# Performance work log

Measured on AMD Instinct MI355X. Metric: run time of the kernel, lower is better.

Reference implementation:

```python
import jax, jax.numpy as jnp
import numpy as np

N, NF, D, H, L, FFN, E, EF = 2048, 64, 256, 8, 6, 1024, 32768, 16
HD = D // H
MAXDEG, MAXDIST = 64, 8


def setup_inputs() -> dict:
    key = jax.random.key(0)
    ks = jax.random.split(key, 32)
    s = 0.02
    nrm = lambda k, sh: (jax.random.normal(k, sh, jnp.float32) * s)
    return {
        "x": jax.random.normal(ks[0], (N, NF), jnp.float32),
        "edge_attr": jax.random.normal(ks[1], (E, EF), jnp.float32),
        "node_proj_w": nrm(ks[2], (D, NF)),
        "node_proj_b": jnp.zeros((D,), jnp.float32),
        "in_deg_emb": nrm(ks[3], (MAXDEG + 1, D)),
        "out_deg_emb": nrm(ks[4], (MAXDEG + 1, D)),
        "dist_bias": nrm(ks[5], (MAXDIST + 2, H)),
        "edge_proj_w": nrm(ks[6], (H, EF)),
        "edge_proj_b": jnp.zeros((H,), jnp.float32),
        "cls_token": nrm(ks[7], (1, D)),
        "q_w": nrm(ks[8], (L, D, D)), "q_b": jnp.zeros((L, D)),
        "k_w": nrm(ks[9], (L, D, D)), "k_b": jnp.zeros((L, D)),
        "v_w": nrm(ks[10], (L, D, D)), "v_b": jnp.zeros((L, D)),
        "o_w": nrm(ks[11], (L, D, D)), "o_b": jnp.zeros((L, D)),
        "ffn1_w": nrm(ks[12], (L, FFN, D)), "ffn1_b": jnp.zeros((L, FFN)),
        "ffn2_w": nrm(ks[13], (L, D, FFN)), "ffn2_b": jnp.zeros((L, D)),
        "ln1_s": jnp.ones((L, D)), "ln1_b": jnp.zeros((L, D)),
        "ln2_s": jnp.ones((L, D)), "ln2_b": jnp.zeros((L, D)),
        "fn_s": jnp.ones((D,)), "fn_b": jnp.zeros((D,)),
        "edge_index": jax.random.randint(ks[14], (2, E), 0, N, dtype=jnp.int32),
        "dist_matrix": jax.random.randint(ks[15], (N, N), 0, MAXDIST + 2, dtype=jnp.int32),
    }


def _ln(v, s, b):
    m = v.mean(-1, keepdims=True)
    va = v.var(-1, keepdims=True)
    return (v - m) / jnp.sqrt(va + 1e-5) * s + b


def _forward(x, edge_attr, node_proj_w, node_proj_b, in_deg_emb, out_deg_emb,
             dist_bias, edge_proj_w, edge_proj_b, cls_token,
             q_w, q_b, k_w, k_b, v_w, v_b, o_w, o_b,
             ffn1_w, ffn1_b, ffn2_w, ffn2_b,
             ln1_s, ln1_b, ln2_s, ln2_b, fn_s, fn_b,
             edge_index, dist_matrix):
    # node embedding + degree encoding
    h = x @ node_proj_w.T + node_proj_b  # (N, D)
    ones = jnp.ones((E,), jnp.int32)
    in_deg = jnp.clip(jax.ops.segment_sum(ones, edge_index[1], num_segments=N), 0, MAXDEG)
    out_deg = jnp.clip(jax.ops.segment_sum(ones, edge_index[0], num_segments=N), 0, MAXDEG)
    h = h + in_deg_emb[in_deg] + out_deg_emb[out_deg]
    h = jnp.concatenate([cls_token, h], axis=0)  # (N+1, D), CLS at row 0
    Nf = N + 1
    # spatial bias: pad dist matrix with zeros for CLS, then embed
    dist_p = jnp.pad(jnp.clip(dist_matrix, 0, MAXDIST + 1), ((1, 0), (1, 0)))
    bias = dist_bias[dist_p]  # (Nf, Nf, H)
    # edge-feature bias: scatter-add projected edge features into dense (N,N,H)
    proj = edge_attr @ edge_proj_w.T + edge_proj_b  # (E, H)
    ebias = jnp.zeros((N, N, H), h.dtype).at[edge_index[0], edge_index[1]].add(proj)
    bias = bias + jnp.pad(ebias, ((1, 0), (1, 0), (0, 0)))
    bias_t = bias.transpose(2, 0, 1)  # (H, Nf, Nf)
    scale = np.sqrt(HD).astype(np.float32)
    for l in range(L):
        hn = _ln(h, ln1_s[l], ln1_b[l])
        Q = (hn @ q_w[l].T + q_b[l]).reshape(Nf, H, HD).transpose(1, 0, 2)
        K = (hn @ k_w[l].T + k_b[l]).reshape(Nf, H, HD).transpose(1, 0, 2)
        V = (hn @ v_w[l].T + v_b[l]).reshape(Nf, H, HD).transpose(1, 0, 2)
        logits = jnp.einsum('hnd,hmd->hnm', Q, K) / scale + bias_t
        attn = jax.nn.softmax(logits, axis=-1)
        o = jnp.einsum('hnm,hmd->hnd', attn, V).transpose(1, 0, 2).reshape(Nf, D)
        h = h + o @ o_w[l].T + o_b[l]
        hn2 = _ln(h, ln2_s[l], ln2_b[l])
        h = h + jax.nn.gelu(hn2 @ ffn1_w[l].T + ffn1_b[l], approximate=False) @ ffn2_w[l].T + ffn2_b[l]
    h = _ln(h, fn_s, fn_b)
    return h, h[0]


def reference(x, edge_attr, node_proj_w, node_proj_b, in_deg_emb, out_deg_emb,
              dist_bias, edge_proj_w, edge_proj_b, cls_token,
              q_w, q_b, k_w, k_b, v_w, v_b, o_w, o_b,
              ffn1_w, ffn1_b, ffn2_w, ffn2_b,
              ln1_s, ln1_b, ln2_s, ln2_b, fn_s, fn_b,
              edge_index, dist_matrix):
    return _forward(x, edge_attr, node_proj_w, node_proj_b, in_deg_emb, out_deg_emb,
                    dist_bias, edge_proj_w, edge_proj_b, cls_token,
                    q_w, q_b, k_w, k_b, v_w, v_b, o_w, o_b,
                    ffn1_w, ffn1_b, ffn2_w, ffn2_b,
                    ln1_s, ln1_b, ln2_s, ln2_b, fn_s, fn_b,
                    edge_index, dist_matrix)
```

## Files before the change

### kernel.cpp

```cpp
#include <hip/hip_runtime.h>
#include <math.h>

#define N_ 2048
#define NF_IN 64
#define D_ 256
#define H_ 8
#define HD_ 32
#define L_ 6
#define FFN_ 1024
#define E_ 32768
#define EF_ 16
#define NF 2049
#define MAXDEG_ 64
#define BSTRIDE 2112
#define RPAD 2112
#define NSPLIT 4
#define LOG2E 1.4426950408889634f

typedef __attribute__((ext_vector_type(8))) short bf16x8;
typedef __attribute__((ext_vector_type(4))) float f32x4;

__device__ inline unsigned short f2b(float f){
  union { float f; unsigned u; } v; v.f = f;
  unsigned r = (v.u + 0x7fffu + ((v.u >> 16) & 1u)) >> 16;
  return (unsigned short)r;
}
__device__ inline float b2f(short s){
  union { unsigned u; float f; } v; v.u = ((unsigned)(unsigned short)s) << 16;
  return v.f;
}

__device__ inline unsigned char f2fp8(float f){
  unsigned u = __float_as_uint(f);
  unsigned s = (u >> 24) & 0x80u;
  float a = fabsf(f);
  if (a >= 448.f) return (unsigned char)(s | 0x7Eu);
  if (a < 0.015625f){
    int k = (int)rintf(a * 512.f);
    return (unsigned char)(s | (unsigned)k);
  }
  int e; float m = frexpf(a, &e);
  int E = e - 1;
  int m3 = (int)rintf(m * 16.f) - 8;
  if (m3 == 8){ E++; m3 = 0; }
  if (E > 8){ E = 8; m3 = 6; }
  if (E == 8 && m3 > 6) m3 = 6;
  return (unsigned char)(s | (unsigned)((E + 7) << 3) | (unsigned)m3);
}
__device__ inline float fp82f(unsigned char b){
  return __builtin_amdgcn_cvt_f32_fp8((int)b, 0);
}

__device__ inline void atomic_add_fp8(unsigned char* p, float add){
  unsigned* wp = (unsigned*)((size_t)p & ~(size_t)3);
  int sh = (int)((size_t)p & 3) * 8;
  unsigned old = *wp, assumed;
  do {
    assumed = old;
    unsigned char cur = (unsigned char)((assumed >> sh) & 0xFFu);
    float f = fp82f(cur) + add;
    unsigned nw = (assumed & ~(0xFFu << sh)) | ((unsigned)f2fp8(f) << sh);
    old = atomicCAS(wp, assumed, nw);
  } while (old != assumed);
}

__device__ inline float wred_sum(float v){
  #pragma unroll
  for (int o = 32; o > 0; o >>= 1) v += __shfl_down(v, o, 64);
  return v;
}

__global__ void zero_int(int* p, int n){
  int i = blockIdx.x * blockDim.x + threadIdx.x;
  if (i < n) p[i] = 0;
}

__global__ void deg_count(const int* __restrict__ ei, int* __restrict__ ind,
                          int* __restrict__ outd){
  int e = blockIdx.x * blockDim.x + threadIdx.x;
  if (e >= E_) return;
  atomicAdd(&outd[ei[e]], 1);
  atomicAdd(&ind[ei[E_ + e]], 1);
}

__global__ void embed_k(const float* __restrict__ x, const float* __restrict__ W,
                        const float* __restrict__ b, const float* __restrict__ inE,
                        const float* __restrict__ outE, const int* __restrict__ ind,
                        const int* __restrict__ outd, const float* __restrict__ cls,
                        float* __restrict__ h){
  int i = blockIdx.x, d = threadIdx.x;
  if (i == 0){ h[d] = cls[d]; return; }
  int n = i - 1;
  const float4* xr = (const float4*)(x + (long)n * NF_IN);
  const float4* wr = (const float4*)(W + (long)d * NF_IN);
  float acc = b[d];
  #pragma unroll
  for (int k = 0; k < NF_IN / 4; k++){
    float4 a = xr[k], w = wr[k];
    acc += a.x * w.x + a.y * w.y + a.z * w.z + a.w * w.w;
  }
  int id = min(ind[n], MAXDEG_), od = min(outd[n], MAXDEG_);
  acc += inE[(long)id * D_ + d] + outE[(long)od * D_ + d];
  h[(long)i * D_ + d] = acc;
}

__global__ void bias_fill(const int* __restrict__ dist, const float* __restrict__ db,
                          unsigned char* __restrict__ bb){
  __shared__ unsigned char lut8[10][H_];
  int i = blockIdx.x;
  if (threadIdx.x < 80)
    ((unsigned char*)lut8)[threadIdx.x] = f2fp8(db[threadIdx.x] * LOG2E);
  __syncthreads();
  for (int u = threadIdx.x; u < BSTRIDE / 8; u += 256){
    int dp[8];
    #pragma unroll
    for (int k = 0; k < 8; k++){
      int j = u * 8 + k;
      int d = 0;
      if (i > 0 && j > 0 && j < NF){
        int dv = dist[(long)(i - 1) * N_ + (j - 1)];
        d = max(0, min(dv, 9));
      }
      dp[k] = (j < NF) ? d : -1;
    }
    #pragma unroll
    for (int h = 0; h < H_; h++){
      unsigned lo = 0, hi = 0;
      #pragma unroll
      for (int k = 0; k < 4; k++){
        unsigned b0 = (dp[k] >= 0) ? lut8[dp[k]][h] : 0u;
        unsigned b1 = (dp[4 + k] >= 0) ? lut8[dp[4 + k]][h] : 0u;
        lo |= b0 << (8 * k);
        hi |= b1 << (8 * k);
      }
      *(uint2*)(bb + ((long)h * NF + i) * BSTRIDE + u * 8) = make_uint2(lo, hi);
    }
  }
}

__global__ void edge_bias(const float* __restrict__ ea, const float* __restrict__ W,
                          const float* __restrict__ b, const int* __restrict__ ei,
                          unsigned char* __restrict__ bb){
  int e = blockIdx.x * blockDim.x + threadIdx.x;
  if (e >= E_) return;
  float a[EF_];
  #pragma unroll
  for (int k = 0; k < EF_; k++) a[k] = ea[(long)e * EF_ + k];
  int src = ei[e], dst = ei[E_ + e];
  #pragma unroll
  for (int h = 0; h < H_; h++){
    float p = b[h];
    #pragma unroll
    for (int k = 0; k < EF_; k++) p += a[k] * W[h * EF_ + k];
    atomic_add_fp8(bb + ((long)h * NF + src + 1) * BSTRIDE + (dst + 1), p * LOG2E);
  }
}

__global__ void w2b_all(const float* __restrict__ qw, const float* __restrict__ kw,
                        const float* __restrict__ vw, const float* __restrict__ ow,
                        const float* __restrict__ f1w, const float* __restrict__ f2w,
                        short* __restrict__ wqkv, short* __restrict__ owb,
                        short* __restrict__ f1wb, short* __restrict__ f2wb){
  long i = (long)blockIdx.x * 256 + threadIdx.x;
  const long DD = (long)D_ * D_, LDD = (long)L_ * DD, LFD = (long)L_ * FFN_ * D_;
  if (i < LDD){
    long l = i / DD, r = i - l * DD;
    wqkv[l * 3 * DD + r]          = (short)f2b(qw[i]);
    wqkv[l * 3 * DD + DD + r]     = (short)f2b(kw[i]);
    wqkv[l * 3 * DD + 2 * DD + r] = (short)f2b(vw[i]);
    owb[i] = (short)f2b(ow[i]);
  }
  if (i < LFD){
    f1wb[i] = (short)f2b(f1w[i]);
    f2wb[i] = (short)f2b(f2w[i]);
  }
}

__global__ void ln_k(const float* __restrict__ in, const float* __restrict__ s,
                     const float* __restrict__ b, float* __restrict__ outf,
                     short* __restrict__ outb, int dup0){
  __shared__ float r1[4], r2[4];
  int i = blockIdx.x, d = threadIdx.x;
  float v = in[(long)i * D_ + d];
  float s1 = wred_sum(v), s2 = wred_sum(v * v);
  if ((d & 63) == 0){ r1[d >> 6] = s1; r2[d >> 6] = s2; }
  __syncthreads();
  float S1 = r1[0] + r1[1] + r1[2] + r1[3];
  float S2 = r2[0] + r2[1] + r2[2] + r2[3];
  float m = S1 * (1.0f / D_);
  float var = S2 * (1.0f / D_) - m * m;
  float y = (v - m) * rsqrtf(var + 1e-5f) * s[d] + b[d];
  if (outf){
    outf[(long)i * D_ + d] = y;
    if (dup0 && i == 0) outf[(long)NF * D_ + d] = y;
  }
  if (outb) outb[(long)i * D_ + d] = (short)f2b(y);
}

__global__ __launch_bounds__(256) void qkv_gemm(const short* __restrict__ A,
    const short* __restrict__ Wall, const float* __restrict__ qb,
    const float* __restrict__ kb, const float* __restrict__ vb,
    short* __restrict__ QKb, short* __restrict__ Vtg, int l){
  const int z = blockIdx.z;
  const short* W = Wall + ((long)(l * 3 + z)) * D_ * D_;
  const float* bsp = (z == 0) ? qb : (z == 1) ? kb : vb;
  __shared__ __align__(16) short As[64][40], Ws[64][40];
  __shared__ __align__(16) short Tt[64][72];
  const int tid = threadIdx.x, lane = tid & 63, wave = tid >> 6;
  const int col = lane & 15, quad = lane >> 4;
  const int wm = wave & 1, wn = wave >> 1;
  const int bm = blockIdx.x * 64, bn = blockIdx.y * 64;
  const f32x4 zero4 = {0.f, 0.f, 0.f, 0.f};
  f32x4 acc[2][2] = {{zero4, zero4}, {zero4, zero4}};
  const int row = tid >> 2, seg = tid & 3;
  for (int k0 = 0; k0 < D_; k0 += 32){
    __syncthreads();
    bf16x8 av = (bf16x8)(short)0;
    int gm = bm + row;
    if (gm < NF) av = *(const bf16x8*)(A + (long)gm * D_ + k0 + seg * 8);
    *(bf16x8*)&As[row][seg * 8] = av;
    *(bf16x8*)&Ws[row][seg * 8] = *(const bf16x8*)(W + (long)(bn + row) * D_ + k0 + seg * 8);
    __syncthreads();
    bf16x8 a0 = *(const bf16x8*)&As[wm * 32 + col][quad * 8];
    bf16x8 a1 = *(const bf16x8*)&As[wm * 32 + 16 + col][quad * 8];
    bf16x8 b0 = *(const bf16x8*)&Ws[wn * 32 + col][quad * 8];
    bf16x8 b1 = *(const bf16x8*)&Ws[wn * 32 + 16 + col][quad * 8];
    acc[0][0] = __builtin_amdgcn_mfma_f32_16x16x32_bf16(a0, b0, acc[0][0], 0, 0, 0);
    acc[0][1] = __builtin_amdgcn_mfma_f32_16x16x32_bf16(a0, b1, acc[0][1], 0, 0, 0);
    acc[1][0] = __builtin_amdgcn_mfma_f32_16x16x32_bf16(a1, b0, acc[1][0], 0, 0, 0);
    acc[1][1] = __builtin_amdgcn_mfma_f32_16x16x32_bf16(a1, b1, acc[1][1], 0, 0, 0);
  }
  if (z < 2){
    const float qscale = 0.25501133194822025f;
    #pragma unroll
    for (int i = 0; i < 2; i++)
      #pragma unroll
      for (int j = 0; j < 2; j++)
        #pragma unroll
        for (int r = 0; r < 4; r++){
          int gm = bm + wm * 32 + i * 16 + quad * 4 + r;
          if (gm >= NF) continue;
          int gn = bn + wn * 32 + j * 16 + col;
          float v = acc[i][j][r] + bsp[gn];
          if (z == 0) v *= qscale;
          QKb[(long)z * NF * D_ + (long)gm * D_ + gn] = (short)f2b(v);
        }
  } else {
    #pragma unroll
    for (int i = 0; i < 2; i++)
      #pragma unroll
      for (int j = 0; j < 2; j++){
        int ln_ = wn * 32 + j * 16 + col;
        int lc = wm * 32 + i * 16 + quad * 4;
        float bsv = bsp[bn + ln_];
        short pk[4];
        #pragma unroll
        for (int r = 0; r < 4; r++) pk[r] = (short)f2b(acc[i][j][r] + bsv);
        *(short4*)&Tt[ln_][lc] = *(short4*)pk;
      }
    __syncthreads();
    int lr = tid >> 2, sg = tid & 3;
    bf16x8 v0 = *(const bf16x8*)&Tt[lr][sg * 16];
    bf16x8 v1 = *(const bf16x8*)&Tt[lr][sg * 16 + 8];
    short* dstp = Vtg + (long)(bn + lr) * BSTRIDE + bm + sg * 16;
    *(bf16x8*)dstp = v0;
    *(bf16x8*)(dstp + 8) = v1;
  }
}

template<int ACT, int ATOM, int MERGE>
__global__ __launch_bounds__(256) void mgemm(const short* __restrict__ A,
    const float* __restrict__ Op, const float* __restrict__ Lp,
    const short* __restrict__ W, const float* __restrict__ bs,
    float* __restrict__ Cf, short* __restrict__ Cb,
    int M, int Nn, int Kc, int Kstride){
  __shared__ __align__(16) short As[64][40], Ws[64][40];
  const int tid = threadIdx.x, lane = tid & 63, wave = tid >> 6;
  const int col = lane & 15, quad = lane >> 4;
  const int wm = wave & 1, wn = wave >> 1;
  const int bm = blockIdx.x * 64, bn = blockIdx.y * 64;
  const int koff = blockIdx.z * Kc;
  const f32x4 zero4 = {0.f, 0.f, 0.f, 0.f};
  f32x4 acc[2][2] = {{zero4, zero4}, {zero4, zero4}};
  const int row = tid >> 2, seg = tid & 3;
  for (int k0 = 0; k0 < Kc; k0 += 32){
    __syncthreads();
    int gm = bm + row;
    if (MERGE){
      int kg = koff + k0 + seg * 8;
      int hh = kg >> 5, d0 = kg & 31;
      short sarr[8] = {0,0,0,0,0,0,0,0};
      if (gm < M){
        float o0=0,o1=0,o2=0,o3=0,o4=0,o5=0,o6=0,o7=0, sl=0.f;
        #pragma unroll
        for (int q = 0; q < NSPLIT; q++){
          long rb = (long)(q * H_ + hh) * RPAD + gm;
          const float* op = Op + rb * HD_ + d0;
          float4 v0 = *(const float4*)op, v1 = *(const float4*)(op + 4);
          o0 += v0.x; o1 += v0.y; o2 += v0.z; o3 += v0.w;
          o4 += v1.x; o5 += v1.y; o6 += v1.z; o7 += v1.w;
          sl += Lp[rb];
        }
        float inv = 1.0f / sl;
        sarr[0]=(short)f2b(o0*inv); sarr[1]=(short)f2b(o1*inv);
        sarr[2]=(short)f2b(o2*inv); sarr[3]=(short)f2b(o3*inv);
        sarr[4]=(short)f2b(o4*inv); sarr[5]=(short)f2b(o5*inv);
        sarr[6]=(short)f2b(o6*inv); sarr[7]=(short)f2b(o7*inv);
      }
      *(bf16x8*)&As[row][seg * 8] = *(bf16x8*)sarr;
    } else {
      bf16x8 av = (bf16x8)(short)0;
      if (gm < M) av = *(const bf16x8*)(A + (long)gm * Kstride + koff + k0 + seg * 8);
      *(bf16x8*)&As[row][seg * 8] = av;
    }
    *(bf16x8*)&Ws[row][seg * 8] =
      *(const bf16x8*)(W + (long)(bn + row) * Kstride + koff + k0 + seg * 8);
    __syncthreads();
    bf16x8 a0 = *(const bf16x8*)&As[wm * 32 + col][quad * 8];
    bf16x8 a1 = *(const bf16x8*)&As[wm * 32 + 16 + col][quad * 8];
    bf16x8 b0 = *(const bf16x8*)&Ws[wn * 32 + col][quad * 8];
    bf16x8 b1 = *(const bf16x8*)&Ws[wn * 32 + 16 + col][quad * 8];
    acc[0][0] = __builtin_amdgcn_mfma_f32_16x16x32_bf16(a0, b0, acc[0][0], 0, 0, 0);
    acc[0][1] = __builtin_amdgcn_mfma_f32_16x16x32_bf16(a0, b1, acc[0][1], 0, 0, 0);
    acc[1][0] = __builtin_amdgcn_mfma_f32_16x16x32_bf16(a1, b0, acc[1][0], 0, 0, 0);
    acc[1][1] = __builtin_amdgcn_mfma_f32_16x16x32_bf16(a1, b1, acc[1][1], 0, 0, 0);
  }
  #pragma unroll
  for (int i = 0; i < 2; i++)
    #pragma unroll
    for (int j = 0; j < 2; j++)
      #pragma unroll
      for (int r = 0; r < 4; r++){
        int gm = bm + wm * 32 + i * 16 + quad * 4 + r;
        if (gm >= M) continue;
        int gn = bn + wn * 32 + j * 16 + col;
        if (ATOM){
          float v = acc[i][j][r] + (blockIdx.z == 0 ? bs[gn] : 0.f);
          atomicAdd(&Cf[(long)gm * Nn + gn], v);
        } else {
          float v = acc[i][j][r] + bs[gn];
          if (ACT == 1) v = v * 0.5f * (1.0f + erff(v * 0.70710678118654752f));
          Cb[(long)gm * Nn + gn] = (short)f2b(v);
        }
      }
}

__global__ __launch_bounds__(256) void fattn_k(const short* __restrict__ Qb,
    const short* __restrict__ Kb, const short* __restrict__ Vtg,
    const unsigned char* __restrict__ bias8, float* __restrict__ Opart,
    float* __restrict__ Lpart){
  __shared__ __align__(16) short Ks[64][42];
  __shared__ __align__(16) short Vt[32][72];
  __shared__ __align__(16) short Ps[4][16][72];

  const int tid = threadIdx.x, wave = tid >> 6, lane = tid & 63;
  const int col = lane & 15, quad = lane >> 4;
  const int h = blockIdx.y, qz = blockIdx.z;
  const int i0 = blockIdx.x * 64 + wave * 16;
  const int t0 = (qz == 0) ? 0 : 9 + 8 * (qz - 1);
  const int t1 = t0 + ((qz == 0) ? 9 : 8);

  int qrow = min(i0 + col, NF - 1);
  bf16x8 qf = *(const bf16x8*)(Qb + (long)qrow * D_ + h * HD_ + quad * 8);

  int brow[4];
  #pragma unroll
  for (int r = 0; r < 4; r++) brow[r] = min(i0 + quad * 4 + r, NF - 1);

  f32x4 oacc0 = {0.f, 0.f, 0.f, 0.f}, oacc1 = {0.f, 0.f, 0.f, 0.f};
  float rs[4] = {0.f, 0.f, 0.f, 0.f};
  const f32x4 zero4 = {0.f, 0.f, 0.f, 0.f};
  short* Pp = &Ps[wave][0][0];

  for (int t = t0; t < t1; t++){
    const int j0 = t * 64;
    unsigned bw[4];
    #pragma unroll
    for (int r = 0; r < 4; r++)
      bw[r] = *(const unsigned*)(bias8 + (long)(h * NF + brow[r]) * BSTRIDE + j0 + col * 4);
    __syncthreads();
    {
      int key = tid >> 2, seg = tid & 3;
      int j = j0 + key;
      bf16x8 kv = (bf16x8)(short)0;
      if (j < NF) kv = *(const bf16x8*)(Kb + (long)j * D_ + h * HD_ + seg * 8);
      *(bf16x8*)&Ks[key][seg * 8] = kv;
    }
    {
      int d = tid >> 3, seg = tid & 7;
      *(bf16x8*)&Vt[d][seg * 8] =
        *(const bf16x8*)(Vtg + (long)(h * HD_ + d) * BSTRIDE + j0 + seg * 8);
    }
    __syncthreads();

    f32x4 sacc[4];
    #pragma unroll
    for (int t4 = 0; t4 < 4; t4++){
      bf16x8 kf = *(const bf16x8*)&Ks[col * 4 + t4][quad * 8];
      sacc[t4] = __builtin_amdgcn_mfma_f32_16x16x32_bf16(qf, kf, zero4, 0, 0, 0);
    }

    const bool tail = (j0 + 64 > NF);
    #pragma unroll
    for (int r = 0; r < 4; r++){
      float bv0 = __builtin_amdgcn_cvt_f32_fp8((int)bw[r], 0);
      float bv1 = __builtin_amdgcn_cvt_f32_fp8((int)bw[r], 1);
      float bv2 = __builtin_amdgcn_cvt_f32_fp8((int)bw[r], 2);
      float bv3 = __builtin_amdgcn_cvt_f32_fp8((int)bw[r], 3);
      float bvv[4] = {bv0, bv1, bv2, bv3};
      unsigned short pb[4];
      #pragma unroll
      for (int t4 = 0; t4 < 4; t4++){
        float p = exp2f(sacc[t4][r] + bvv[t4]);
        if (tail && (j0 + col * 4 + t4 >= NF)) p = 0.f;
        unsigned pu = __float_as_uint(p) & 0xffff0000u;
        rs[r] += __uint_as_float(pu);
        pb[t4] = (unsigned short)(pu >> 16);
      }
      unsigned u0 = (unsigned)pb[0] | ((unsigned)pb[1] << 16);
      unsigned u1 = (unsigned)pb[2] | ((unsigned)pb[3] << 16);
      *(uint2*)&Pp[(quad * 4 + r) * 72 + col * 4] = make_uint2(u0, u1);
    }

    #pragma unroll
    for (int ks = 0; ks < 2; ks++){
      bf16x8 af = *(const bf16x8*)&Pp[col * 72 + ks * 32 + quad * 8];
      bf16x8 v0 = *(const bf16x8*)&Vt[col][ks * 32 + quad * 8];
      bf16x8 v1 = *(const bf16x8*)&Vt[16 + col][ks * 32 + quad * 8];
      oacc0 = __builtin_amdgcn_mfma_f32_16x16x32_bf16(af, v0, oacc0, 0, 0, 0);
      oacc1 = __builtin_amdgcn_mfma_f32_16x16x32_bf16(af, v1, oacc1, 0, 0, 0);
    }
  }

  #pragma unroll
  for (int r = 0; r < 4; r++){
    #pragma unroll
    for (int o = 1; o < 16; o <<= 1) rs[r] += __shfl_xor(rs[r], o, 64);
  }
  long pi = ((long)qz * H_ + h) * RPAD + i0 + quad * 4;
  #pragma unroll
  for (int r = 0; r < 4; r++){
    Opart[(pi + r) * HD_ + col] = oacc0[r];
    Opart[(pi + r) * HD_ + 16 + col] = oacc1[r];
    if (col == 0) Lpart[pi + r] = rs[r];
  }
}

extern "C" void kernel_launch(void* const* d_in, const int* in_sizes, int n_in,
                              void* d_out, int out_size, void* d_ws, size_t ws_size,
                              hipStream_t stream){
  const float* x    = (const float*)d_in[0];
  const float* ea   = (const float*)d_in[1];
  const float* npw  = (const float*)d_in[2];
  const float* npb  = (const float*)d_in[3];
  const float* inE  = (const float*)d_in[4];
  const float* outE = (const float*)d_in[5];
  const float* db   = (const float*)d_in[6];
  const float* epw  = (const float*)d_in[7];
  const float* epb  = (const float*)d_in[8];
  const float* cls  = (const float*)d_in[9];
  const float* qw   = (const float*)d_in[10];
  const float* qb   = (const float*)d_in[11];
  const float* kw   = (const float*)d_in[12];
  const float* kb   = (const float*)d_in[13];
  const float* vw   = (const float*)d_in[14];
  const float* vb   = (const float*)d_in[15];
  const float* ow   = (const float*)d_in[16];
  const float* ob   = (const float*)d_in[17];
  const float* f1w  = (const float*)d_in[18];
  const float* f1b  = (const float*)d_in[19];
  const float* f2w  = (const float*)d_in[20];
  const float* f2bp = (const float*)d_in[21];
  const float* ln1s = (const float*)d_in[22];
  const float* ln1b = (const float*)d_in[23];
  const float* ln2s = (const float*)d_in[24];
  const float* ln2b = (const float*)d_in[25];
  const float* fns  = (const float*)d_in[26];
  const float* fnb  = (const float*)d_in[27];
  const int*   ei   = (const int*)d_in[28];
  const int*   dist = (const int*)d_in[29];

  float* ws = (float*)d_ws;
  long off = 0;
  float* h     = ws + off; off += (long)NF * D_;
  float* Opart = ws + off; off += (long)NSPLIT * H_ * RPAD * HD_;
  float* Lpart = ws + off; off += (long)NSPLIT * H_ * RPAD;
  unsigned char* bias8 = (unsigned char*)(ws + off);
  off += ((long)H_ * NF * BSTRIDE + 3) / 4;
  short* hnb   = (short*)(ws + off); off += ((long)NF * D_ + 1) / 2;
  short* QKb   = (short*)(ws + off); off += (long)NF * D_;
  short* Vtg   = (short*)(ws + off); off += ((long)D_ * BSTRIDE + 1) / 2;
  short* midb  = (short*)(ws + off); off += ((long)NF * FFN_ + 1) / 2;
  short* wqkv  = (short*)(ws + off); off += ((long)3 * L_ * D_ * D_ + 1) / 2;
  short* owb   = (short*)(ws + off); off += ((long)L_ * D_ * D_ + 1) / 2;
  short* f1wb  = (short*)(ws + off); off += ((long)L_ * FFN_ * D_ + 1) / 2;
  short* f2wb  = (short*)(ws + off); off += ((long)L_ * FFN_ * D_ + 1) / 2;
  int*   ind   = (int*)(ws + off);
  int*   outd  = ind + N_;

  zero_int<<<(2 * N_ + 255) / 256, 256, 0, stream>>>(ind, 2 * N_);
  deg_count<<<(E_ + 255) / 256, 256, 0, stream>>>(ei, ind, outd);
  embed_k<<<NF, D_, 0, stream>>>(x, npw, npb, inE, outE, ind, outd, cls, h);
  bias_fill<<<NF, 256, 0, stream>>>(dist, db, bias8);
  edge_bias<<<(E_ + 255) / 256, 256, 0, stream>>>(ea, epw, epb, ei, bias8);
  {
    long LFD = (long)L_ * FFN_ * D_;
    w2b_all<<<(int)((LFD + 255) / 256), 256, 0, stream>>>(qw, kw, vw, ow, f1w, f2w,
                                                          wqkv, owb, f1wb, f2wb);
  }

  dim3 gQKV((NF + 63) / 64, D_ / 64, 3);
  dim3 gO((NF + 63) / 64, D_ / 64, 2);
  dim3 gF((NF + 63) / 64, FFN_ / 64, 1);
  dim3 gF2((NF + 63) / 64, D_ / 64, 4);
  dim3 gA((NF + 63) / 64, H_, NSPLIT);
  for (int l = 0; l < L_; l++){
    ln_k<<<NF, D_, 0, stream>>>(h, ln1s + l * D_, ln1b + l * D_, nullptr, hnb, 0);
    qkv_gemm<<<gQKV, 256, 0, stream>>>(hnb, wqkv, qb + l * D_, kb + l * D_, vb + l * D_,
                                       QKb, Vtg, l);
    fattn_k<<<gA, 256, 0, stream>>>(QKb, QKb + (long)NF * D_, Vtg, bias8, Opart, Lpart);
    mgemm<0,1,1><<<gO, 256, 0, stream>>>(nullptr, Opart, Lpart,
                                         owb + (long)l * D_ * D_, ob + l * D_,
                                         h, nullptr, NF, D_, 128, D_);
    ln_k<<<NF, D_, 0, stream>>>(h, ln2s + l * D_, ln2b + l * D_, nullptr, hnb, 0);
    mgemm<1,0,0><<<gF, 256, 0, stream>>>(hnb, nullptr, nullptr,
                                         f1wb + (long)l * FFN_ * D_, f1b + l * FFN_,
                                         nullptr, midb, NF, FFN_, D_, D_);
    mgemm<0,1,0><<<gF2, 256, 0, stream>>>(midb, nullptr, nullptr,
                                          f2wb + (long)l * FFN_ * D_, f2bp + l * D_,
                                          h, nullptr, NF, D_, 256, FFN_);
  }
  ln_k<<<NF, D_, 0, stream>>>(h, fns, fnb, (float*)d_out, nullptr, 1);
}
```

Measured before the change: 684.7 us.

## Double-buffer GEMM and attention tiles, vectorize layernorm, compute row sums via MFMA

The QKV, generic and attention kernels now keep two LDS buffers and stage the next K-tile (or K/V tile) while MFMAs run on the current one, leaving one barrier per iteration. Layernorm handles four rows per block, one wave per row, using float4 loads and xor-shuffle reductions with no shared memory. In attention, the softmax row sums come from an extra MFMA against a vector of ones instead of scalar accumulation and shuffles, and the tail masking moves into a separate branch. The double buffers raise LDS use per block, which may lower occupancy, and the ones-MFMA adds matrix-core work per tile.

```diff
diff --git a/kernel.cpp b/kernel.cpp
--- a/kernel.cpp
+++ b/kernel.cpp
@@ -64,12 +64,6 @@
   } while (old != assumed);
 }
 
-__device__ inline float wred_sum(float v){
-  #pragma unroll
-  for (int o = 32; o > 0; o >>= 1) v += __shfl_down(v, o, 64);
-  return v;
-}
-
 __global__ void zero_int(int* p, int n){
   int i = blockIdx.x * blockDim.x + threadIdx.x;
   if (i < n) p[i] = 0;
@@ -176,25 +170,41 @@
   }
 }
 
-__global__ void ln_k(const float* __restrict__ in, const float* __restrict__ s,
-                     const float* __restrict__ b, float* __restrict__ outf,
-                     short* __restrict__ outb, int dup0){
-  __shared__ float r1[4], r2[4];
-  int i = blockIdx.x, d = threadIdx.x;
-  float v = in[(long)i * D_ + d];
-  float s1 = wred_sum(v), s2 = wred_sum(v * v);
-  if ((d & 63) == 0){ r1[d >> 6] = s1; r2[d >> 6] = s2; }
-  __syncthreads();
-  float S1 = r1[0] + r1[1] + r1[2] + r1[3];
-  float S2 = r2[0] + r2[1] + r2[2] + r2[3];
-  float m = S1 * (1.0f / D_);
-  float var = S2 * (1.0f / D_) - m * m;
-  float y = (v - m) * rsqrtf(var + 1e-5f) * s[d] + b[d];
+__global__ __launch_bounds__(256) void ln_k(const float* __restrict__ in,
+                     const float* __restrict__ s, const float* __restrict__ b,
+                     float* __restrict__ outf, short* __restrict__ outb,
+                     int dup0, int M){
+  int row = blockIdx.x * 4 + (threadIdx.x >> 6);
+  int lane = threadIdx.x & 63;
+  if (row >= M) return;
+  float4 v = *(const float4*)(in + (long)row * D_ + lane * 4);
+  float s1 = v.x + v.y + v.z + v.w;
+  float s2 = v.x * v.x + v.y * v.y + v.z * v.z + v.w * v.w;
+  #pragma unroll
+  for (int o = 1; o < 64; o <<= 1){
+    s1 += __shfl_xor(s1, o, 64);
+    s2 += __shfl_xor(s2, o, 64);
+  }
+  float m = s1 * (1.0f / D_);
+  float var = s2 * (1.0f / D_) - m * m;
+  float rstd = rsqrtf(var + 1e-5f);
+  float4 sc = *(const float4*)(s + lane * 4);
+  float4 bb = *(const float4*)(b + lane * 4);
+  float y0 = (v.x - m) * rstd * sc.x + bb.x;
+  float y1 = (v.y - m) * rstd * sc.y + bb.y;
+  float y2 = (v.z - m) * rstd * sc.z + bb.z;
+  float y3 = (v.w - m) * rstd * sc.w + bb.w;
   if (outf){
-    outf[(long)i * D_ + d] = y;
-    if (dup0 && i == 0) outf[(long)NF * D_ + d] = y;
-  }
-  if (outb) outb[(long)i * D_ + d] = (short)f2b(y);
+    float4 o4 = make_float4(y0, y1, y2, y3);
+    *(float4*)(outf + (long)row * D_ + lane * 4) = o4;
+    if (dup0 && row == 0) *(float4*)(outf + (long)NF * D_ + lane * 4) = o4;
+  }
+  if (outb){
+    short4 pk;
+    pk.x = (short)f2b(y0); pk.y = (short)f2b(y1);
+    pk.z = (short)f2b(y2); pk.w = (short)f2b(y3);
+    *(short4*)(outb + (long)row * D_ + lane * 4) = pk;
+  }
 }
 
 __global__ __launch_bounds__(256) void qkv_gemm(const short* __restrict__ A,
@@ -204,7 +214,7 @@
   const int z = blockIdx.z;
   const short* W = Wall + ((long)(l * 3 + z)) * D_ * D_;
   const float* bsp = (z == 0) ? qb : (z == 1) ? kb : vb;
-  __shared__ __align__(16) short As[64][40], Ws[64][40];
+  __shared__ __align__(16) short As[2][64][40], Ws[2][64][40];
   __shared__ __align__(16) short Tt[64][72];
   const int tid = threadIdx.x, lane = tid & 63, wave = tid >> 6;
   const int col = lane & 15, quad = lane >> 4;
@@ -213,22 +223,30 @@
   const f32x4 zero4 = {0.f, 0.f, 0.f, 0.f};
   f32x4 acc[2][2] = {{zero4, zero4}, {zero4, zero4}};
   const int row = tid >> 2, seg = tid & 3;
-  for (int k0 = 0; k0 < D_; k0 += 32){
-    __syncthreads();
+
+  auto stage = [&](int buf, int k0){
     bf16x8 av = (bf16x8)(short)0;
     int gm = bm + row;
     if (gm < NF) av = *(const bf16x8*)(A + (long)gm * D_ + k0 + seg * 8);
-    *(bf16x8*)&As[row][seg * 8] = av;
-    *(bf16x8*)&Ws[row][seg * 8] = *(const bf16x8*)(W + (long)(bn + row) * D_ + k0 + seg * 8);
+    *(bf16x8*)&As[buf][row][seg * 8] = av;
+    *(bf16x8*)&Ws[buf][row][seg * 8] =
+      *(const bf16x8*)(W + (long)(bn + row) * D_ + k0 + seg * 8);
+  };
+
+  stage(0, 0);
+  int cur = 0;
+  for (int k0 = 0; k0 < D_; k0 += 32){
     __syncthreads();
-    bf16x8 a0 = *(const bf16x8*)&As[wm * 32 + col][quad * 8];
-    bf16x8 a1 = *(const bf16x8*)&As[wm * 32 + 16 + col][quad * 8];
-    bf16x8 b0 = *(const bf16x8*)&Ws[wn * 32 + col][quad * 8];
-    bf16x8 b1 = *(const bf16x8*)&Ws[wn * 32 + 16 + col][quad * 8];
+    if (k0 + 32 < D_) stage(cur ^ 1, k0 + 32);
+    bf16x8 a0 = *(const bf16x8*)&As[cur][wm * 32 + col][quad * 8];
+    bf16x8 a1 = *(const bf16x8*)&As[cur][wm * 32 + 16 + col][quad * 8];
+    bf16x8 b0 = *(const bf16x8*)&Ws[cur][wn * 32 + col][quad * 8];
+    bf16x8 b1 = *(const bf16x8*)&Ws[cur][wn * 32 + 16 + col][quad * 8];
     acc[0][0] = __builtin_amdgcn_mfma_f32_16x16x32_bf16(a0, b0, acc[0][0], 0, 0, 0);
     acc[0][1] = __builtin_amdgcn_mfma_f32_16x16x32_bf16(a0, b1, acc[0][1], 0, 0, 0);
     acc[1][0] = __builtin_amdgcn_mfma_f32_16x16x32_bf16(a1, b0, acc[1][0], 0, 0, 0);
     acc[1][1] = __builtin_amdgcn_mfma_f32_16x16x32_bf16(a1, b1, acc[1][1], 0, 0, 0);
+    cur ^= 1;
   }
   if (z < 2){
     const float qscale = 0.25501133194822025f;
@@ -274,7 +292,7 @@
     const short* __restrict__ W, const float* __restrict__ bs,
     float* __restrict__ Cf, short* __restrict__ Cb,
     int M, int Nn, int Kc, int Kstride){
-  __shared__ __align__(16) short As[64][40], Ws[64][40];
+  __shared__ __align__(16) short As[2][64][40], Ws[2][64][40];
   const int tid = threadIdx.x, lane = tid & 63, wave = tid >> 6;
   const int col = lane & 15, quad = lane >> 4;
   const int wm = wave & 1, wn = wave >> 1;
@@ -283,8 +301,8 @@
   const f32x4 zero4 = {0.f, 0.f, 0.f, 0.f};
   f32x4 acc[2][2] = {{zero4, zero4}, {zero4, zero4}};
   const int row = tid >> 2, seg = tid & 3;
-  for (int k0 = 0; k0 < Kc; k0 += 32){
-    __syncthreads();
+
+  auto stage = [&](int buf, int k0){
     int gm = bm + row;
     if (MERGE){
       int kg = koff + k0 + seg * 8;
@@ -307,23 +325,31 @@
         sarr[4]=(short)f2b(o4*inv); sarr[5]=(short)f2b(o5*inv);
         sarr[6]=(short)f2b(o6*inv); sarr[7]=(short)f2b(o7*inv);
       }
-      *(bf16x8*)&As[row][seg * 8] = *(bf16x8*)sarr;
+      *(bf16x8*)&As[buf][row][seg * 8] = *(bf16x8*)sarr;
     } else {
       bf16x8 av = (bf16x8)(short)0;
       if (gm < M) av = *(const bf16x8*)(A + (long)gm * Kstride + koff + k0 + seg * 8);
-      *(bf16x8*)&As[row][seg * 8] = av;
-    }
-    *(bf16x8*)&Ws[row][seg * 8] =
+      *(bf16x8*)&As[buf][row][seg * 8] = av;
+    }
+    *(bf16x8*)&Ws[buf][row][seg * 8] =
       *(const bf16x8*)(W + (long)(bn + row) * Kstride + koff + k0 + seg * 8);
+  };
+
+  stage(0, 0);
+  const int nk = Kc >> 5;
+  int cur = 0;
+  for (int i = 0; i < nk; i++){
     __syncthreads();
-    bf16x8 a0 = *(const bf16x8*)&As[wm * 32 + col][quad * 8];
-    bf16x8 a1 = *(const bf16x8*)&As[wm * 32 + 16 + col][quad * 8];
-    bf16x8 b0 = *(const bf16x8*)&Ws[wn * 32 + col][quad * 8];
-    bf16x8 b1 = *(const bf16x8*)&Ws[wn * 32 + 16 + col][quad * 8];
+    if (i + 1 < nk) stage(cur ^ 1, (i + 1) << 5);
+    bf16x8 a0 = *(const bf16x8*)&As[cur][wm * 32 + col][quad * 8];
+    bf16x8 a1 = *(const bf16x8*)&As[cur][wm * 32 + 16 + col][quad * 8];
+    bf16x8 b0 = *(const bf16x8*)&Ws[cur][wn * 32 + col][quad * 8];
+    bf16x8 b1 = *(const bf16x8*)&Ws[cur][wn * 32 + 16 + col][quad * 8];
     acc[0][0] = __builtin_amdgcn_mfma_f32_16x16x32_bf16(a0, b0, acc[0][0], 0, 0, 0);
     acc[0][1] = __builtin_amdgcn_mfma_f32_16x16x32_bf16(a0, b1, acc[0][1], 0, 0, 0);
     acc[1][0] = __builtin_amdgcn_mfma_f32_16x16x32_bf16(a1, b0, acc[1][0], 0, 0, 0);
     acc[1][1] = __builtin_amdgcn_mfma_f32_16x16x32_bf16(a1, b1, acc[1][1], 0, 0, 0);
+    cur ^= 1;
   }
   #pragma unroll
   for (int i = 0; i < 2; i++)
@@ -349,8 +375,8 @@
     const short* __restrict__ Kb, const short* __restrict__ Vtg,
     const unsigned char* __restrict__ bias8, float* __restrict__ Opart,
     float* __restrict__ Lpart){
-  __shared__ __align__(16) short Ks[64][42];
-  __shared__ __align__(16) short Vt[32][72];
+  __shared__ __align__(16) short Ks[2][64][42];
+  __shared__ __align__(16) short Vt[2][32][72];
   __shared__ __align__(16) short Ps[4][16][72];
 
   const int tid = threadIdx.x, wave = tid >> 6, lane = tid & 63;
@@ -368,81 +394,97 @@
   for (int r = 0; r < 4; r++) brow[r] = min(i0 + quad * 4 + r, NF - 1);
 
   f32x4 oacc0 = {0.f, 0.f, 0.f, 0.f}, oacc1 = {0.f, 0.f, 0.f, 0.f};
-  float rs[4] = {0.f, 0.f, 0.f, 0.f};
+  f32x4 racc = {0.f, 0.f, 0.f, 0.f};
   const f32x4 zero4 = {0.f, 0.f, 0.f, 0.f};
+  const bf16x8 ones8 = (bf16x8)(short)0x3F80;
   short* Pp = &Ps[wave][0][0];
 
-  for (int t = t0; t < t1; t++){
-    const int j0 = t * 64;
-    unsigned bw[4];
-    #pragma unroll
-    for (int r = 0; r < 4; r++)
-      bw[r] = *(const unsigned*)(bias8 + (long)(h * NF + brow[r]) * BSTRIDE + j0 + col * 4);
-    __syncthreads();
+  auto stageKV = [&](int buf, int t){
+    int j0 = t * 64;
     {
       int key = tid >> 2, seg = tid & 3;
       int j = j0 + key;
       bf16x8 kv = (bf16x8)(short)0;
       if (j < NF) kv = *(const bf16x8*)(Kb + (long)j * D_ + h * HD_ + seg * 8);
-      *(bf16x8*)&Ks[key][seg * 8] = kv;
+      *(bf16x8*)&Ks[buf][key][seg * 8] = kv;
     }
     {
       int d = tid >> 3, seg = tid & 7;
-      *(bf16x8*)&Vt[d][seg * 8] =
+      *(bf16x8*)&Vt[buf][d][seg * 8] =
         *(const bf16x8*)(Vtg + (long)(h * HD_ + d) * BSTRIDE + j0 + seg * 8);
     }
+  };
+
+  stageKV(0, t0);
+  int cur = 0;
+  for (int t = t0; t < t1; t++){
+    const int j0 = t * 64;
+    unsigned bw[4];
+    #pragma unroll
+    for (int r = 0; r < 4; r++)
+      bw[r] = *(const unsigned*)(bias8 + (long)(h * NF + brow[r]) * BSTRIDE + j0 + col * 4);
     __syncthreads();
+    if (t + 1 < t1) stageKV(cur ^ 1, t + 1);
 
     f32x4 sacc[4];
     #pragma unroll
     for (int t4 = 0; t4 < 4; t4++){
-      bf16x8 kf = *(const bf16x8*)&Ks[col * 4 + t4][quad * 8];
+      bf16x8 kf = *(const bf16x8*)&Ks[cur][col * 4 + t4][quad * 8];
       sacc[t4] = __builtin_amdgcn_mfma_f32_16x16x32_bf16(qf, kf, zero4, 0, 0, 0);
     }
 
-    const bool tail = (j0 + 64 > NF);
-    #pragma unroll
-    for (int r = 0; r < 4; r++){
-      float bv0 = __builtin_amdgcn_cvt_f32_fp8((int)bw[r], 0);
-      float bv1 = __builtin_amdgcn_cvt_f32_fp8((int)bw[r], 1);
-      float bv2 = __builtin_amdgcn_cvt_f32_fp8((int)bw[r], 2);
-      float bv3 = __builtin_amdgcn_cvt_f32_fp8((int)bw[r], 3);
-      float bvv[4] = {bv0, bv1, bv2, bv3};
-      unsigned short pb[4];
+    if (j0 + 64 > NF){
       #pragma unroll
-      for (int t4 = 0; t4 < 4; t4++){
-        float p = exp2f(sacc[t4][r] + bvv[t4]);
-        if (tail && (j0 + col * 4 + t4 >= NF)) p = 0.f;
-        unsigned pu = __float_as_uint(p) & 0xffff0000u;
-        rs[r] += __uint_as_float(pu);
-        pb[t4] = (unsigned short)(pu >> 16);
-      }
-      unsigned u0 = (unsigned)pb[0] | ((unsigned)pb[1] << 16);
-      unsigned u1 = (unsigned)pb[2] | ((unsigned)pb[3] << 16);
-      *(uint2*)&Pp[(quad * 4 + r) * 72 + col * 4] = make_uint2(u0, u1);
+      for (int r = 0; r < 4; r++){
+        unsigned w = bw[r];
+        float s0 = sacc[0][r] + __builtin_amdgcn_cvt_f32_fp8((int)w, 0);
+        float s1 = sacc[1][r] + __builtin_amdgcn_cvt_f32_fp8((int)w, 1);
+        float s2 = sacc[2][r] + __builtin_amdgcn_cvt_f32_fp8((int)w, 2);
+        float s3 = sacc[3][r] + __builtin_amdgcn_cvt_f32_fp8((int)w, 3);
+        unsigned p0 = (j0 + col * 4 + 0 < NF) ? __float_as_uint(exp2f(s0)) : 0u;
+        unsigned p1 = (j0 + col * 4 + 1 < NF) ? __float_as_uint(exp2f(s1)) : 0u;
+        unsigned p2 = (j0 + col * 4 + 2 < NF) ? __float_as_uint(exp2f(s2)) : 0u;
+        unsigned p3 = (j0 + col * 4 + 3 < NF) ? __float_as_uint(exp2f(s3)) : 0u;
+        unsigned u0 = (p0 >> 16) | (p1 & 0xffff0000u);
+        unsigned u1 = (p2 >> 16) | (p3 & 0xffff0000u);
+        *(uint2*)&Pp[(quad * 4 + r) * 72 + col * 4] = make_uint2(u0, u1);
+      }
+    } else {
+      #pragma unroll
+      for (int r = 0; r < 4; r++){
+        unsigned w = bw[r];
+        float s0 = sacc[0][r] + __builtin_amdgcn_cvt_f32_fp8((int)w, 0);
+        float s1 = sacc[1][r] + __builtin_amdgcn_cvt_f32_fp8((int)w, 1);
+        float s2 = sacc[2][r] + __builtin_amdgcn_cvt_f32_fp8((int)w, 2);
+        float s3 = sacc[3][r] + __builtin_amdgcn_cvt_f32_fp8((int)w, 3);
+        unsigned p0 = __float_as_uint(exp2f(s0));
+        unsigned p1 = __float_as_uint(exp2f(s1));
+        unsigned p2 = __float_as_uint(exp2f(s2));
+        unsigned p3 = __float_as_uint(exp2f(s3));
+        unsigned u0 = (p0 >> 16) | (p1 & 0xffff0000u);
+        unsigned u1 = (p2 >> 16) | (p3 & 0xffff0000u);
+        *(uint2*)&Pp[(quad * 4 + r) * 72 + col * 4] = make_uint2(u0, u1);
+      }
     }
 
     #pragma unroll
     for (int ks = 0; ks < 2; ks++){
       bf16x8 af = *(const bf16x8*)&Pp[col * 72 + ks * 32 + quad * 8];
-      bf16x8 v0 = *(const bf16x8*)&Vt[col][ks * 32 + quad * 8];
-      bf16x8 v1 = *(const bf16x8*)&Vt[16 + col][ks * 32 + quad * 8];
+      bf16x8 v0 = *(const bf16x8*)&Vt[cur][col][ks * 32 + quad * 8];
+      bf16x8 v1 = *(const bf16x8*)&Vt[cur][16 + col][ks * 32 + quad * 8];
       oacc0 = __builtin_amdgcn_mfma_f32_16x16x32_bf16(af, v0, oacc0, 0, 0, 0);
       oacc1 = __builtin_amdgcn_mfma_f32_16x16x32_bf16(af, v1, oacc1, 0, 0, 0);
-    }
-  }
-
-  #pragma unroll
-  for (int r = 0; r < 4; r++){
-    #pragma unroll
-    for (int o = 1; o < 16; o <<= 1) rs[r] += __shfl_xor(rs[r], o, 64);
-  }
+      racc  = __builtin_amdgcn_mfma_f32_16x16x32_bf16(af, ones8, racc, 0, 0, 0);
+    }
+    cur ^= 1;
+  }
+
   long pi = ((long)qz * H_ + h) * RPAD + i0 + quad * 4;
   #pragma unroll
   for (int r = 0; r < 4; r++){
     Opart[(pi + r) * HD_ + col] = oacc0[r];
     Opart[(pi + r) * HD_ + 16 + col] = oacc1[r];
-    if (col == 0) Lpart[pi + r] = rs[r];
+    if (col == 0) Lpart[pi + r] = racc[r];
   }
 }
 
@@ -509,20 +551,21 @@
                                                           wqkv, owb, f1wb, f2wb);
   }
 
+  const int gLN = (NF + 3) / 4;
   dim3 gQKV((NF + 63) / 64, D_ / 64, 3);
   dim3 gO((NF + 63) / 64, D_ / 64, 2);
   dim3 gF((NF + 63) / 64, FFN_ / 64, 1);
   dim3 gF2((NF + 63) / 64, D_ / 64, 4);
   dim3 gA((NF + 63) / 64, H_, NSPLIT);
   for (int l = 0; l < L_; l++){
-    ln_k<<<NF, D_, 0, stream>>>(h, ln1s + l * D_, ln1b + l * D_, nullptr, hnb, 0);
+    ln_k<<<gLN, 256, 0, stream>>>(h, ln1s + l * D_, ln1b + l * D_, nullptr, hnb, 0, NF);
     qkv_gemm<<<gQKV, 256, 0, stream>>>(hnb, wqkv, qb + l * D_, kb + l * D_, vb + l * D_,
                                        QKb, Vtg, l);
     fattn_k<<<gA, 256, 0, stream>>>(QKb, QKb + (long)NF * D_, Vtg, bias8, Opart, Lpart);
     mgemm<0,1,1><<<gO, 256, 0, stream>>>(nullptr, Opart, Lpart,
                                          owb + (long)l * D_ * D_, ob + l * D_,
                                          h, nullptr, NF, D_, 128, D_);
-    ln_k<<<NF, D_, 0, stream>>>(h, ln2s + l * D_, ln2b + l * D_, nullptr, hnb, 0);
+    ln_k<<<gLN, 256, 0, stream>>>(h, ln2s + l * D_, ln2b + l * D_, nullptr, hnb, 0, NF);
     mgemm<1,0,0><<<gF, 256, 0, stream>>>(hnb, nullptr, nullptr,
                                          f1wb + (long)l * FFN_ * D_, f1b + l * FFN_,
                                          nullptr, midb, NF, FFN_, D_, D_);
@@ -530,5 +573,5 @@
                                           f2wb + (long)l * FFN_ * D_, f2bp + l * D_,
                                           h, nullptr, NF, D_, 256, FFN_);
   }
-  ln_k<<<NF, D_, 0, stream>>>(h, fns, fnb, (float*)d_out, nullptr, 1);
-}
+  ln_k<<<gLN, 256, 0, stream>>>(h, fns, fnb, (float*)d_out, nullptr, 1, NF);
+}
```

After: 657.8 us. -3.9%, faster.
